# Kernel optimization log

Measured on AMD Instinct MI355X. Metric: run time of the kernel, lower is better.

Reference implementation:

```python
import jax, jax.numpy as jnp
import numpy as np

H_IMG, W_IMG = 256, 256
FX = FY = 300.0
CX, CY = W_IMG / 2.0, H_IMG / 2.0
NEAR, FAR = 0.01, 100.0
MAX_RADIUS = 64.0
N_GAUSS = 4096


def quat_to_rot(q):
    q = q / jnp.linalg.norm(q, axis=-1, keepdims=True)
    w, x, y, z = q[..., 0], q[..., 1], q[..., 2], q[..., 3]
    R = jnp.stack([
        1 - 2 * y * y - 2 * z * z, 2 * x * y - 2 * w * z, 2 * x * z + 2 * w * y,
        2 * x * y + 2 * w * z, 1 - 2 * x * x - 2 * z * z, 2 * y * z - 2 * w * x,
        2 * x * z - 2 * w * y, 2 * y * z + 2 * w * x, 1 - 2 * x * x - 2 * y * y,
    ], axis=-1)
    return R.reshape(q.shape[:-1] + (3, 3))


def setup_inputs():
    key = jax.random.key(0)
    k1, k2, k3, k4, k5, k6 = jax.random.split(key, 6)
    xy = jax.random.normal(k1, (N_GAUSS, 2), jnp.float32) * 2.0
    z = -(jax.random.uniform(k2, (N_GAUSS, 1), jnp.float32) * 6.0 + 2.0)  # depths in [2, 8]
    positions = jnp.concatenate([xy, z], axis=1)
    scales = jax.random.uniform(k3, (N_GAUSS, 3), jnp.float32) * 0.10 + 0.02
    rotations = jax.random.normal(k4, (N_GAUSS, 4), jnp.float32)
    colors = jax.random.uniform(k5, (N_GAUSS, 3), jnp.float32)
    opacities = jax.random.uniform(k6, (N_GAUSS,), jnp.float32) * 0.8 + 0.1
    view_matrix = jnp.eye(4, dtype=jnp.float32)
    return {"positions": positions, "scales": scales, "rotations": rotations,
            "colors": colors, "opacities": opacities, "view_matrix": view_matrix}


def _render(positions, scales, rotations, colors, opacities, view_matrix):
    N = positions.shape[0]
    pts = jnp.concatenate([positions, jnp.ones((N, 1), positions.dtype)], axis=1)
    pc = (view_matrix @ pts.T).T[:, :3]  # camera-space points (N,3)
    x, y, z = pc[:, 0], pc[:, 1], pc[:, 2]
    depths = -z
    z_safe = jnp.clip(jnp.abs(z), 0.01) * jnp.sign(z + 1e-8)
    z2 = z_safe * z_safe
    # 3D covariance = (Rcam R S)(Rcam R S)^T
    R = quat_to_rot(rotations)
    R_cam = view_matrix[:3, :3] @ R
    RS = R_cam * scales[:, None, :]  # right-multiply by diag(scales)
    cov3d = RS @ jnp.swapaxes(RS, -1, -2)
    # perspective Jacobian (N,2,3)
    zr = jnp.zeros_like(x)
    J = jnp.stack([
        jnp.stack([FX / -z_safe, zr, FX * x / z2], axis=-1),
        jnp.stack([zr, FY / z_safe, FY * y / z2], axis=-1),
    ], axis=-2)
    cov2d = J @ cov3d @ jnp.swapaxes(J, -1, -2)
    u = FX * x / -z_safe + CX
    v = FY * -y / -z_safe + CY
    # effective radius: 3 sigma from max eigenvalue of 2x2 covariance
    a, b = cov2d[:, 0, 0], cov2d[:, 0, 1]
    c, d = cov2d[:, 1, 0], cov2d[:, 1, 1]
    tr = a + d
    det = jnp.clip(a * d - b * c, 1e-6)
    disc = jnp.clip(tr * tr - 4.0 * det, 0.0)
    lam = (tr + jnp.sqrt(disc)) * 0.5
    radii = jnp.minimum(3.0 * jnp.sqrt(jnp.clip(lam, 1e-6)), MAX_RADIUS)
    # depth sort (front to back)
    order = jnp.argsort(depths)
    u, v, a, b, c, d = u[order], v[order], a[order], b[order], c[order], d[order]
    radii, depths = radii[order], depths[order]
    colors_s, op_s = colors[order], opacities[order]
    # visibility culling: zero opacity instead of compaction (same math, static shapes)
    visible = (depths > NEAR) & (depths < FAR)
    visible &= (u + radii > 0) & (u - radii < W_IMG)
    visible &= (v + radii > 0) & (v - radii < H_IMG)
    op_s = jnp.where(visible, op_s, 0.0)
    # regularized 2x2 inverse (pinv of PD matrix == inverse)
    ar, dr = a + 1e-4, d + 1e-4
    inv_det = 1.0 / (ar * dr - b * c)
    ia, ib, ic, idd = dr * inv_det, -b * inv_det, -c * inv_det, ar * inv_det
    px = jnp.arange(W_IMG, dtype=jnp.float32)[None, :]
    py = jnp.arange(H_IMG, dtype=jnp.float32)[:, None]

    def step(carry, g):
        acc_c, acc_a = carry
        mx, my, gia, gib, gic, gid, r, col, o = g
        dx = px - mx  # (1,W)
        dy = py - my  # (H,1)
        power = -0.5 * (gia * dx * dx + (gib + gic) * dx * dy + gid * dy * dy)
        # bounding-box mask replicating the torch tile bounds [int(m-r), int(m+r)+1)
        inside = ((px >= jnp.trunc(mx - r)) & (px <= jnp.trunc(mx + r))
                  & (py >= jnp.trunc(my - r)) & (py <= jnp.trunc(my + r)))
        alpha = jnp.where(inside, o * jnp.exp(power), 0.0)
        w = alpha * (1.0 - acc_a)  # front-to-back over-compositing
        return (acc_c + w[..., None] * col, acc_a + w), None

    acc0 = (jnp.zeros((H_IMG, W_IMG, 3), jnp.float32),
            jnp.zeros((H_IMG, W_IMG), jnp.float32))
    (acc_c, acc_a), _ = jax.lax.scan(
        step, acc0, (u, v, ia, ib, ic, idd, radii, colors_s, op_s))
    bg = jnp.zeros(3, jnp.float32)
    img = acc_c + (1.0 - acc_a)[..., None] * bg
    return jnp.transpose(img, (2, 0, 1))  # (3,H,W)


def reference(positions, scales, rotations, colors, opacities, view_matrix):
    return _render(positions, scales, rotations, colors, opacities, view_matrix)
```

## Files before the change

### kernel.cpp

```cpp
#include <hip/hip_runtime.h>
#include <hip/hip_fp16.h>
#include <math.h>

#define N_G   4096
#define CAP   1024
#define W_IMG 256
#define H_IMG 256

__global__ __launch_bounds__(256) void prep(
    const float* __restrict__ pos, const float* __restrict__ scl,
    const float* __restrict__ rot, const float* __restrict__ col,
    const float* __restrict__ opa, const float* __restrict__ vm,
    float4* __restrict__ gaussU, short4* __restrict__ bbhU,
    float* __restrict__ depthU)
{
  const int i = blockIdx.x * 256 + threadIdx.x;
  if (i >= N_G) return;
  const float FX=300.f, FY=300.f, CXc=128.f, CYc=128.f;
  const float HLOG2E = 0.72134752f;
  float V00=vm[0],V01=vm[1],V02=vm[2],V03=vm[3];
  float V10=vm[4],V11=vm[5],V12=vm[6],V13=vm[7];
  float V20=vm[8],V21=vm[9],V22=vm[10],V23=vm[11];
  float p0=pos[3*i], p1=pos[3*i+1], p2=pos[3*i+2];
  float X = V00*p0+V01*p1+V02*p2+V03;
  float Y = V10*p0+V11*p1+V12*p2+V13;
  float Z = V20*p0+V21*p1+V22*p2+V23;
  float depth = -Z;
  float zp = Z + 1e-8f;
  float sgn = (zp>0.f)?1.f:((zp<0.f)?-1.f:0.f);
  float z_safe = fmaxf(fabsf(Z), 0.01f) * sgn;
  float z2 = z_safe*z_safe;
  float qw=rot[4*i], qx=rot[4*i+1], qy=rot[4*i+2], qz=rot[4*i+3];
  float qi = 1.f/sqrtf(qw*qw+qx*qx+qy*qy+qz*qz);
  qw*=qi; qx*=qi; qy*=qi; qz*=qi;
  float R00=1.f-2.f*qy*qy-2.f*qz*qz, R01=2.f*qx*qy-2.f*qw*qz, R02=2.f*qx*qz+2.f*qw*qy;
  float R10=2.f*qx*qy+2.f*qw*qz, R11=1.f-2.f*qx*qx-2.f*qz*qz, R12=2.f*qy*qz-2.f*qw*qx;
  float R20=2.f*qx*qz-2.f*qw*qy, R21=2.f*qy*qz+2.f*qw*qx, R22=1.f-2.f*qx*qx-2.f*qy*qy;
  float C00=V00*R00+V01*R10+V02*R20, C01=V00*R01+V01*R11+V02*R21, C02=V00*R02+V01*R12+V02*R22;
  float C10=V10*R00+V11*R10+V12*R20, C11=V10*R01+V11*R11+V12*R21, C12=V10*R02+V11*R12+V12*R22;
  float C20=V20*R00+V21*R10+V22*R20, C21=V20*R01+V21*R11+V22*R21, C22=V20*R02+V21*R12+V22*R22;
  float s0=scl[3*i], s1=scl[3*i+1], s2=scl[3*i+2];
  float S00=C00*s0,S01=C01*s1,S02=C02*s2;
  float S10=C10*s0,S11=C11*s1,S12=C12*s2;
  float S20=C20*s0,S21=C21*s1,S22=C22*s2;
  float c00=S00*S00+S01*S01+S02*S02;
  float c01=S00*S10+S01*S11+S02*S12;
  float c02=S00*S20+S01*S21+S02*S22;
  float c11=S10*S10+S11*S11+S12*S12;
  float c12=S10*S20+S11*S21+S12*S22;
  float c22=S20*S20+S21*S21+S22*S22;
  float j00=FX/(-z_safe), j02=FX*X/z2;
  float j11=FY/z_safe,    j12=FY*Y/z2;
  float M00=j00*c00+j02*c02, M01=j00*c01+j02*c12, M02=j00*c02+j02*c22;
  float M10=j11*c01+j12*c02, M11=j11*c11+j12*c12, M12=j11*c12+j12*c22;
  float a =M00*j00+M02*j02;
  float b =M01*j11+M02*j12;
  float c_=M10*j00+M12*j02;
  float d =M11*j11+M12*j12;
  float u = FX*X/(-z_safe)+CXc;
  float v = FY*(-Y)/(-z_safe)+CYc;
  float tr=a+d;
  float det=fmaxf(a*d-b*c_, 1e-6f);
  float disc=fmaxf(tr*tr-4.f*det, 0.f);
  float lam=(tr+sqrtf(disc))*0.5f;
  float radius=fminf(3.f*sqrtf(fmaxf(lam,1e-6f)), 64.f);
  bool vis = (depth>0.01f)&&(depth<100.f)
          && (u+radius>0.f)&&(u-radius<(float)W_IMG)
          && (v+radius>0.f)&&(v-radius<(float)H_IMG);
  float o = vis ? opa[i] : 0.f;
  float ar=a+1e-4f, dr=d+1e-4f;
  float inv=1.f/(ar*dr-b*c_);
  short4 bb = make_short4(1000, -1000, 1000, -1000);
  if (o>0.f) {
    bb.x=(short)truncf(u-radius); bb.y=(short)truncf(u+radius);
    bb.z=(short)truncf(v-radius); bb.w=(short)truncf(v+radius);
  }
  unsigned hrg = (unsigned)__half_as_ushort(__float2half_rn(col[3*i]))
               | ((unsigned)__half_as_ushort(__float2half_rn(col[3*i+1]))<<16);
  depthU[i] = depth;
  bbhU[i]   = bb;
  gaussU[2*i]   = make_float4(u, v, (dr*inv)*HLOG2E,
                              ((-b*inv)+(-c_*inv))*HLOG2E);
  gaussU[2*i+1] = make_float4((ar*inv)*HLOG2E, log2f(o),
                              __uint_as_float(hrg), col[3*i+2]);
}

__global__ __launch_bounds__(1024) void render(
    const short4* __restrict__ bbhU, const float4* __restrict__ gaussU,
    const float* __restrict__ depthU, float* __restrict__ out)
{
  __shared__ __align__(16) unsigned long long keys[CAP];
  __shared__ float4 gp[CAP*2];
  __shared__ short4 bbh[CAP];
  __shared__ float4 res[16][64];
  __shared__ int lcnt;

  const int tid = threadIdx.x, wv = tid>>6, lane = tid&63;
  const int bid = (int)((blockIdx.x * 331u) & 511u);
  const int RX0=(bid&15)*16, RY0=(bid>>4)*8;
  const int RX1=RX0+15, RY1=RY0+7;

  if (tid==0) lcnt=0;
  __syncthreads();

  {
    short4 bb[4];
    #pragma unroll
    for (int c4=0;c4<4;c4++) bb[c4]=bbhU[(wv*4+c4)*64+lane];
    #pragma unroll
    for (int c4=0;c4<4;c4++) {
      int idx=(wv*4+c4)*64+lane;
      bool pred=(bb[c4].y>=RX0)&&(bb[c4].x<=RX1)&&(bb[c4].w>=RY0)&&(bb[c4].z<=RY1);
      unsigned long long m=__ballot(pred);
      if (m) {
        int bse=0;
        if (lane==0) bse=atomicAdd(&lcnt, __popcll(m));
        bse=__shfl(bse,0);
        if (pred) {
          int p=bse+__popcll(m&((1ull<<lane)-1ull));
          if (p<CAP)
            keys[p]=((unsigned long long)__float_as_uint(depthU[idx])<<12)
                   |(unsigned)idx;
        }
      }
    }
  }
  __syncthreads();
  const int len = (lcnt<CAP)?lcnt:CAP;

  if (tid<len) {
    unsigned long long kj=keys[tid];
    int r=0;
    const ulonglong2* k2=(const ulonglong2*)keys;
    int n2=len>>1;
    for(int s2=0;s2<n2;s2++){
      ulonglong2 kv=k2[s2];
      r += (kv.x<kj)+(kv.y<kj);
    }
    if(len&1) r += (keys[len-1]<kj);
    int idx=(int)(kj&4095u);
    gp[2*r]  =gaussU[2*idx];
    gp[2*r+1]=gaussU[2*idx+1];
    bbh[r]   =bbhU[idx];
  }
  __syncthreads();

  const int t=wv>>3, seg=wv&7;
  const int TX0=RX0+t*8, TY0=RY0, TX1=TX0+7, TY1=TY0+7;
  const int ipx=TX0+(lane&7), ipy=TY0+(lane>>3);
  const float px=(float)ipx, py=(float)ipy;
  const int segLen=(len+7)>>3;
  const int s=seg*segLen;
  int e=s+segLen; if(e>len) e=len;
  float aR=0.f,aG=0.f,aB=0.f,aA=0.f;
  for(int k0=s;k0<e;k0+=64){
    int kk=k0+lane;
    bool ok=false;
    if(kk<e){
      short4 bb=bbh[kk];
      ok=(bb.y>=TX0)&&(bb.x<=TX1)&&(bb.w>=TY0)&&(bb.z<=TY1);
    }
    unsigned long long mm=__ballot(ok);
    if(mm){
      int k=k0+__builtin_ctzll(mm); mm&=mm-1;
      short4 bb=bbh[k];
      float4 A=gp[2*k], B=gp[2*k+1];
      while(mm){
        int kn=k0+__builtin_ctzll(mm); mm&=mm-1;
        short4 bbn=bbh[kn];
        float4 An=gp[2*kn], Bn=gp[2*kn+1];
        float dx=px-A.x, dy=py-A.y;
        float q2=A.z*dx*dx + A.w*dx*dy + B.x*dy*dy;
        bool inside=(ipx>=bb.x)&&(ipx<=bb.y)&&(ipy>=bb.z)&&(ipy<=bb.w);
        float ex=__builtin_amdgcn_exp2f(B.y-q2);
        float alpha= inside ? ex : 0.f;
        float w=alpha*(1.f-aA);
        unsigned hrg=__float_as_uint(B.z);
        float cR=__half2float(__ushort_as_half((unsigned short)(hrg&0xFFFFu)));
        float cG=__half2float(__ushort_as_half((unsigned short)(hrg>>16)));
        aR+=w*cR; aG+=w*cG; aB+=w*B.w; aA+=w;
        bb=bbn; A=An; B=Bn;
      }
      float dx=px-A.x, dy=py-A.y;
      float q2=A.z*dx*dx + A.w*dx*dy + B.x*dy*dy;
      bool inside=(ipx>=bb.x)&&(ipx<=bb.y)&&(ipy>=bb.z)&&(ipy<=bb.w);
      float ex=__builtin_amdgcn_exp2f(B.y-q2);
      float alpha= inside ? ex : 0.f;
      float w=alpha*(1.f-aA);
      unsigned hrg=__float_as_uint(B.z);
      float cR=__half2float(__ushort_as_half((unsigned short)(hrg&0xFFFFu)));
      float cG=__half2float(__ushort_as_half((unsigned short)(hrg>>16)));
      aR+=w*cR; aG+=w*cG; aB+=w*B.w; aA+=w;
    }
    if(__ballot(aA<=0.9999f)==0ull) break;
  }
  res[wv][lane]=make_float4(aR,aG,aB,aA);
  __syncthreads();

  if(seg==0){
    float4 P=res[wv][lane];
    #pragma unroll
    for(int w=1;w<8;w++){
      float4 Q=res[wv+w][lane];
      float tr_=1.f-P.w;
      P.x+=tr_*Q.x; P.y+=tr_*Q.y; P.z+=tr_*Q.z; P.w+=tr_*Q.w;
    }
    out[0*H_IMG*W_IMG + ipy*W_IMG + ipx]=P.x;
    out[1*H_IMG*W_IMG + ipy*W_IMG + ipx]=P.y;
    out[2*H_IMG*W_IMG + ipy*W_IMG + ipx]=P.z;
  }
}

extern "C" void kernel_launch(void* const* d_in, const int* in_sizes, int n_in,
                              void* d_out, int out_size, void* d_ws, size_t ws_size,
                              hipStream_t stream)
{
  const float* pos=(const float*)d_in[0];
  const float* scl=(const float*)d_in[1];
  const float* rot=(const float*)d_in[2];
  const float* col=(const float*)d_in[3];
  const float* opa=(const float*)d_in[4];
  const float* vm =(const float*)d_in[5];
  float* out=(float*)d_out;
  char* ws=(char*)d_ws;
  float4* gaussU=(float4*)(ws);
  short4* bbhU  =(short4*)(ws + 128*1024);
  float*  depthU=(float*) (ws + 160*1024);
  prep<<<N_G/256, 256, 0, stream>>>(pos,scl,rot,col,opa,vm,gaussU,bbhU,depthU);
  render<<<512, 1024, 0, stream>>>(bbhU,gaussU,depthU,out);
}
```

Measured before the change: 19.24 us.

## Shrink render tiles to 8x8 per block and drop per-wave ballot culling

Each render block now covers a single 8x8 pixel tile with 512 threads (8 waves), and the grid doubles to 1024 blocks. The per-block Gaussian list is culled against that exact tile, so the inner loop walks the sorted segment directly without the 64-wide ballot and bounding-box filtering. The early-termination ballot now runs only every 32 Gaussians. The block-level culling and rank sort are repeated for twice as many blocks, with each wave scanning 8 chunks of bounding boxes, so the gain from tighter lists is offset by more redundant list building.

```diff
diff --git a/kernel.cpp b/kernel.cpp
--- a/kernel.cpp
+++ b/kernel.cpp
@@ -85,32 +85,32 @@
                               __uint_as_float(hrg), col[3*i+2]);
 }
 
-__global__ __launch_bounds__(1024) void render(
+__global__ __launch_bounds__(512) void render(
     const short4* __restrict__ bbhU, const float4* __restrict__ gaussU,
     const float* __restrict__ depthU, float* __restrict__ out)
 {
   __shared__ __align__(16) unsigned long long keys[CAP];
   __shared__ float4 gp[CAP*2];
   __shared__ short4 bbh[CAP];
-  __shared__ float4 res[16][64];
+  __shared__ float4 res[8][64];
   __shared__ int lcnt;
 
   const int tid = threadIdx.x, wv = tid>>6, lane = tid&63;
-  const int bid = (int)((blockIdx.x * 331u) & 511u);
-  const int RX0=(bid&15)*16, RY0=(bid>>4)*8;
-  const int RX1=RX0+15, RY1=RY0+7;
+  const int bid = (int)((blockIdx.x * 331u) & 1023u);
+  const int TX0=(bid&31)*8, TY0=(bid>>5)*8;
+  const int TX1=TX0+7, TY1=TY0+7;
 
   if (tid==0) lcnt=0;
   __syncthreads();
 
   {
-    short4 bb[4];
+    short4 bb[8];
     #pragma unroll
-    for (int c4=0;c4<4;c4++) bb[c4]=bbhU[(wv*4+c4)*64+lane];
+    for (int c8=0;c8<8;c8++) bb[c8]=bbhU[(wv*8+c8)*64+lane];
     #pragma unroll
-    for (int c4=0;c4<4;c4++) {
-      int idx=(wv*4+c4)*64+lane;
-      bool pred=(bb[c4].y>=RX0)&&(bb[c4].x<=RX1)&&(bb[c4].w>=RY0)&&(bb[c4].z<=RY1);
+    for (int c8=0;c8<8;c8++) {
+      int idx=(wv*8+c8)*64+lane;
+      bool pred=(bb[c8].y>=TX0)&&(bb[c8].x<=TX1)&&(bb[c8].w>=TY0)&&(bb[c8].z<=TY1);
       unsigned long long m=__ballot(pred);
       if (m) {
         int bse=0;
@@ -145,42 +145,19 @@
   }
   __syncthreads();
 
-  const int t=wv>>3, seg=wv&7;
-  const int TX0=RX0+t*8, TY0=RY0, TX1=TX0+7, TY1=TY0+7;
   const int ipx=TX0+(lane&7), ipy=TY0+(lane>>3);
   const float px=(float)ipx, py=(float)ipy;
   const int segLen=(len+7)>>3;
-  const int s=seg*segLen;
+  const int s=wv*segLen;
   int e=s+segLen; if(e>len) e=len;
   float aR=0.f,aG=0.f,aB=0.f,aA=0.f;
-  for(int k0=s;k0<e;k0+=64){
-    int kk=k0+lane;
-    bool ok=false;
-    if(kk<e){
-      short4 bb=bbh[kk];
-      ok=(bb.y>=TX0)&&(bb.x<=TX1)&&(bb.w>=TY0)&&(bb.z<=TY1);
-    }
-    unsigned long long mm=__ballot(ok);
-    if(mm){
-      int k=k0+__builtin_ctzll(mm); mm&=mm-1;
-      short4 bb=bbh[k];
-      float4 A=gp[2*k], B=gp[2*k+1];
-      while(mm){
-        int kn=k0+__builtin_ctzll(mm); mm&=mm-1;
-        short4 bbn=bbh[kn];
-        float4 An=gp[2*kn], Bn=gp[2*kn+1];
-        float dx=px-A.x, dy=py-A.y;
-        float q2=A.z*dx*dx + A.w*dx*dy + B.x*dy*dy;
-        bool inside=(ipx>=bb.x)&&(ipx<=bb.y)&&(ipy>=bb.z)&&(ipy<=bb.w);
-        float ex=__builtin_amdgcn_exp2f(B.y-q2);
-        float alpha= inside ? ex : 0.f;
-        float w=alpha*(1.f-aA);
-        unsigned hrg=__float_as_uint(B.z);
-        float cR=__half2float(__ushort_as_half((unsigned short)(hrg&0xFFFFu)));
-        float cG=__half2float(__ushort_as_half((unsigned short)(hrg>>16)));
-        aR+=w*cR; aG+=w*cG; aB+=w*B.w; aA+=w;
-        bb=bbn; A=An; B=Bn;
-      }
+  if (s<e) {
+    short4 bb=bbh[s];
+    float4 A=gp[2*s], B=gp[2*s+1];
+    for(int k=s;k<e;k++){
+      int kn=(k+1<e)?(k+1):k;
+      short4 bbn=bbh[kn];
+      float4 An=gp[2*kn], Bn=gp[2*kn+1];
       float dx=px-A.x, dy=py-A.y;
       float q2=A.z*dx*dx + A.w*dx*dy + B.x*dy*dy;
       bool inside=(ipx>=bb.x)&&(ipx<=bb.y)&&(ipy>=bb.z)&&(ipy<=bb.w);
@@ -191,17 +168,18 @@
       float cR=__half2float(__ushort_as_half((unsigned short)(hrg&0xFFFFu)));
       float cG=__half2float(__ushort_as_half((unsigned short)(hrg>>16)));
       aR+=w*cR; aG+=w*cG; aB+=w*B.w; aA+=w;
-    }
-    if(__ballot(aA<=0.9999f)==0ull) break;
+      bb=bbn; A=An; B=Bn;
+      if(!(k&31) && __ballot(aA<=0.9999f)==0ull) break;
+    }
   }
   res[wv][lane]=make_float4(aR,aG,aB,aA);
   __syncthreads();
 
-  if(seg==0){
-    float4 P=res[wv][lane];
+  if(wv==0){
+    float4 P=res[0][lane];
     #pragma unroll
     for(int w=1;w<8;w++){
-      float4 Q=res[wv+w][lane];
+      float4 Q=res[w][lane];
       float tr_=1.f-P.w;
       P.x+=tr_*Q.x; P.y+=tr_*Q.y; P.z+=tr_*Q.z; P.w+=tr_*Q.w;
     }
@@ -227,5 +205,5 @@
   short4* bbhU  =(short4*)(ws + 128*1024);
   float*  depthU=(float*) (ws + 160*1024);
   prep<<<N_G/256, 256, 0, stream>>>(pos,scl,rot,col,opa,vm,gaussU,bbhU,depthU);
-  render<<<512, 1024, 0, stream>>>(bbhU,gaussU,depthU,out);
+  render<<<1024, 512, 0, stream>>>(bbhU,gaussU,depthU,out);
 }
```

Result: slower. 27.63 us (+43.6%).
